# Kernel optimization log

Hardware: AMD Instinct MI355X
Metric: run time of the kernel (lower is better)

Reference implementation:

```python
import jax, jax.numpy as jnp
import numpy as np

B, N, D = 4, 8192, 3
BIG = 1e9  # large finite value to invalidate masked points in min-reduction

def setup_inputs() -> dict:
    key = jax.random.key(0)
    k1, k2, k3, k4 = jax.random.split(key, 4)
    pred = jax.random.normal(k1, (B, N, D), jnp.float32) * 0.05
    target = jax.random.normal(k2, (B, N, D), jnp.float32) * 0.05
    points = jax.random.normal(k3, (B, N, D), jnp.float32)
    mask = jax.random.randint(k4, (B, N), 0, 2).astype(jnp.int32)
    return {"pred": pred, "target": target, "mask": mask, "points": points}

def reference(pred, target, mask, points):
    m = mask.astype(pred.dtype)  # [B, N]
    # masked L1 term: per-point mean over coords, masked mean over all points
    l1 = jnp.abs(pred - target).mean(-1)          # [B, N]
    l1 = (l1 * m).sum() / m.sum()
    # Chamfer between clean and predicted denoised points (squared L2, pytorch3d norm=2)
    clean = points + target                        # [B, N, 3]
    predp = points + pred                          # [B, N, 3]
    d2 = (jnp.sum(clean * clean, -1)[:, :, None]
          + jnp.sum(predp * predp, -1)[:, None, :]
          - 2.0 * jnp.einsum('bnd,bmd->bnm', clean, predp))  # [B, N, N]
    d2 = jnp.maximum(d2, 0.0)
    inv = (1.0 - m) * BIG                          # [B, N], penalty for masked-out points
    min_x = jnp.min(d2 + inv[:, None, :], axis=2)  # [B, N] nearest pred point for each clean
    min_y = jnp.min(d2 + inv[:, :, None], axis=1)  # [B, N] nearest clean point for each pred
    count = jnp.maximum(m.sum(-1), 1.0)            # valid points per batch
    cham = (min_x * m).sum(-1) / count + (min_y * m).sum(-1) / count  # [B]
    cd = cham.sum() / B
    return 0.5 * (l1 + cd)
```

## Files before the change

### kernel.cpp

```cpp
#include <hip/hip_runtime.h>
#include <stdint.h>

#define NPTS 8192
#define BATCH 4
#define CHUNK 512

typedef __attribute__((ext_vector_type(8))) short bf16x8;
typedef __attribute__((ext_vector_type(16))) float f32x16;

struct Accum {
  float l1sum;
  float count[BATCH];
  float minsum[8];
  float pad[3];
};

__device__ __forceinline__ unsigned short f2bf(float x) {
  union { float f; unsigned u; } v; v.f = x;
  unsigned r = v.u + 0x7FFFu + ((v.u >> 16) & 1u);
  return (unsigned short)(r >> 16);
}
__device__ __forceinline__ float bf2f(unsigned short h) {
  union { float f; unsigned u; } v; v.u = ((unsigned)h) << 16;
  return v.f;
}

using as1_t = __attribute__((address_space(1))) const unsigned int;
using as3_t = __attribute__((address_space(3))) unsigned int;
__device__ __forceinline__ void lds_load16(const void* g, void* l) {
  __builtin_amdgcn_global_load_lds((as1_t*)g, (as3_t*)l, 16, 0, 0);
}

__device__ __forceinline__ void writeA(uint4* P, int T, int n,
                                       float x, float y, float z, float nn) {
  float ax = -2.f * x, ay = -2.f * y, az = -2.f * z;
  unsigned xh = f2bf(ax), xl = f2bf(ax - bf2f(xh));
  unsigned yh = f2bf(ay), yl = f2bf(ay - bf2f(yh));
  unsigned zh = f2bf(az), zl = f2bf(az - bf2f(zh));
  unsigned nh = f2bf(nn);
  float rem = nn - bf2f((unsigned short)nh);
  unsigned nm = f2bf(rem);
  unsigned nl = f2bf(rem - bf2f((unsigned short)nm));
  uint4 h0, h1;
  h0.x = xh | (xh << 16); h0.y = xl | (xl << 16);
  h0.z = yh | (yh << 16); h0.w = yl | (yl << 16);
  h1.x = zh | (zh << 16); h1.y = zl | (zl << 16);
  h1.z = nh | (nm << 16); h1.w = nl;
  P[T * 64 + n] = h0;
  P[T * 64 + 32 + n] = h1;
}
__device__ __forceinline__ void writeB(uint4* P, int T, int n,
                                       float x, float y, float z) {
  unsigned xh = f2bf(x), xl = f2bf(x - bf2f((unsigned short)xh));
  unsigned yh = f2bf(y), yl = f2bf(y - bf2f((unsigned short)yh));
  unsigned zh = f2bf(z), zl = f2bf(z - bf2f((unsigned short)zh));
  const unsigned ONE = 0x3F80u;
  unsigned ux = xh | (xl << 16), uy = yh | (yl << 16), uz = zh | (zl << 16);
  uint4 h0, h1;
  h0.x = ux; h0.y = ux; h0.z = uy; h0.w = uy;
  h1.x = uz; h1.y = uz; h1.z = ONE | (ONE << 16); h1.w = ONE;
  P[T * 64 + n] = h0;
  P[T * 64 + 32 + n] = h1;
}

__global__ __launch_bounds__(256) void prep_kernel(
    const float* __restrict__ pred, const float* __restrict__ target,
    const int* __restrict__ mask, const float* __restrict__ points,
    uint4* __restrict__ Apred, uint4* __restrict__ Aclean,
    uint4* __restrict__ Bclean, uint4* __restrict__ Bpred,
    float* __restrict__ qnClean, float* __restrict__ qnPred,
    float* __restrict__ l1part, Accum* __restrict__ acc) {
  int tid = threadIdx.x;
  int g = blockIdx.x * 256 + tid;
  if (g < 16) ((float*)acc)[g] = 0.f;
  float px = pred[3 * g], py = pred[3 * g + 1], pz = pred[3 * g + 2];
  float tx = target[3 * g], ty = target[3 * g + 1], tz = target[3 * g + 2];
  float ox = points[3 * g], oy = points[3 * g + 1], oz = points[3 * g + 2];
  int m = mask[g];
  float cx = ox + tx, cy = oy + ty, cz = oz + tz;
  float qx = ox + px, qy = oy + py, qz = oz + pz;
  float cn = cx * cx + cy * cy + cz * cz;
  float qn = qx * qx + qy * qy + qz * qz;
  float pen = m ? 0.f : 1e9f;
  qnClean[g] = cn;
  qnPred[g] = qn;
  int T = g >> 5, n = g & 31;
  writeA(Apred, T, n, qx, qy, qz, qn + pen);
  writeA(Aclean, T, n, cx, cy, cz, cn + pen);
  writeB(Bclean, T, n, cx, cy, cz);
  writeB(Bpred, T, n, qx, qy, qz);

  float fm = (float)m;
  float l1c = fm * (fabsf(px - tx) + fabsf(py - ty) + fabsf(pz - tz)) * (1.f / 3.f);
  for (int off = 32; off; off >>= 1) l1c += __shfl_down(l1c, off);
  __shared__ float pl[4];
  if ((tid & 63) == 0) pl[tid >> 6] = l1c;
  __syncthreads();
  if (tid == 0) l1part[blockIdx.x] = pl[0] + pl[1] + pl[2] + pl[3];
}

__global__ __launch_bounds__(256) void chamfer_kernel(
    const uint4* __restrict__ Apred, const uint4* __restrict__ Aclean,
    const uint4* __restrict__ Bclean, const uint4* __restrict__ Bpred,
    const float* __restrict__ qnClean, const float* __restrict__ qnPred,
    float* __restrict__ partial) {
  __shared__ uint4 Asm[1024];
  int z = blockIdx.z, dir = z >> 2, b = z & 3;
  const uint4* __restrict__ Ag = dir ? Aclean : Apred;
  const uint4* __restrict__ Bg = dir ? Bpred : Bclean;
  const float* __restrict__ qn = dir ? qnPred : qnClean;
  int jx = blockIdx.x, jbase = jx * CHUNK;
  int qbase = blockIdx.y * CHUNK;
  int tid = threadIdx.x;

  const uint4* Agp = Ag + (size_t)(b * NPTS + jbase) * 2;
#pragma unroll
  for (int it = 0; it < 4; it++) lds_load16(Agp + it * 256 + tid, &Asm[it * 256 + tid]);

  int lane = tid & 63, w = tid >> 6, n = lane & 31;
  const bf16x8* Bb = (const bf16x8*)(Bg + (size_t)(b * NPTS + qbase) * 2);
  bf16x8 bfr[4];
  float acc[4];
#pragma unroll
  for (int q = 0; q < 4; q++) {
    bfr[q] = Bb[(w * 4 + q) * 64 + lane];
    acc[q] = 1e30f;
  }
  __syncthreads();

  const bf16x8* Al = (const bf16x8*)Asm;
  f32x16 zacc = {0.f, 0.f, 0.f, 0.f, 0.f, 0.f, 0.f, 0.f,
                 0.f, 0.f, 0.f, 0.f, 0.f, 0.f, 0.f, 0.f};

#pragma unroll 4
  for (int p = 0; p < 16; p++) {
    bf16x8 af = Al[p * 64 + lane];
#pragma unroll
    for (int q = 0; q < 4; q++) {
      f32x16 d = __builtin_amdgcn_mfma_f32_32x32x16_bf16(af, bfr[q], zacc, 0, 0, 0);
      acc[q] = fminf(fminf(d[0], d[1]), acc[q]);
      acc[q] = fminf(fminf(d[2], d[3]), acc[q]);
      acc[q] = fminf(fminf(d[4], d[5]), acc[q]);
      acc[q] = fminf(fminf(d[6], d[7]), acc[q]);
      acc[q] = fminf(fminf(d[8], d[9]), acc[q]);
      acc[q] = fminf(fminf(d[10], d[11]), acc[q]);
      acc[q] = fminf(fminf(d[12], d[13]), acc[q]);
      acc[q] = fminf(fminf(d[14], d[15]), acc[q]);
    }
  }

  float* __restrict__ Pq = partial + ((size_t)(z * 16 + jx)) * NPTS + qbase;
#pragma unroll
  for (int q = 0; q < 4; q++) {
    float v = fminf(acc[q], __shfl_xor(acc[q], 32));
    int qi = (w * 4 + q) * 32 + n;
    if (lane < 32) Pq[qi] = fmaxf(v + qn[b * NPTS + qbase + qi], 0.f);
  }
}

__global__ __launch_bounds__(256) void reduce_kernel(
    const int* __restrict__ mask, const float* __restrict__ partial,
    Accum* __restrict__ acc) {
  int slice = blockIdx.x >> 3, sub = blockIdx.x & 7;
  int dir = slice >> 2, bb = slice & 3;
  int t = threadIdx.x;
  const float* __restrict__ P = partial + (size_t)slice * 16 * NPTS + sub * 1024;
  float s = 0.f, c = 0.f;
  for (int i = t; i < 1024; i += 256) {
    float v = P[i];
#pragma unroll
    for (int jxx = 1; jxx < 16; jxx++) v = fminf(v, P[jxx * NPTS + i]);
    float m = (float)mask[bb * NPTS + sub * 1024 + i];
    s += m * v;
    c += m;
  }
  for (int off = 32; off; off >>= 1) {
    s += __shfl_down(s, off);
    c += __shfl_down(c, off);
  }
  __shared__ float rs[4], rc[4];
  int wave = t >> 6;
  if ((t & 63) == 0) { rs[wave] = s; rc[wave] = c; }
  __syncthreads();
  if (t == 0) {
    atomicAdd(&acc->minsum[slice], rs[0] + rs[1] + rs[2] + rs[3]);
    if (dir == 0) atomicAdd(&acc->count[bb], rc[0] + rc[1] + rc[2] + rc[3]);
  }
}

__global__ void final_kernel(const Accum* __restrict__ acc,
                             const float* __restrict__ l1part,
                             float* __restrict__ out) {
  int t = threadIdx.x;
  float l1 = l1part[t];
  for (int off = 32; off; off >>= 1) l1 += __shfl_down(l1, off);
  __shared__ float r[2];
  if ((t & 63) == 0) r[t >> 6] = l1;
  __syncthreads();
  if (t == 0) {
    float l1s = r[0] + r[1];
    float msum = 0.f, cham = 0.f;
#pragma unroll
    for (int b = 0; b < BATCH; b++) {
      msum += acc->count[b];
      cham += (acc->minsum[b] + acc->minsum[4 + b]) / fmaxf(acc->count[b], 1.f);
    }
    out[0] = 0.5f * (l1s / msum + cham * (1.f / BATCH));
  }
}

extern "C" void kernel_launch(void* const* d_in, const int* in_sizes, int n_in,
                              void* d_out, int out_size, void* d_ws, size_t ws_size,
                              hipStream_t stream) {
  const float* pred   = (const float*)d_in[0];
  const float* target = (const float*)d_in[1];
  const int*   mask   = (const int*)d_in[2];
  const float* points = (const float*)d_in[3];
  float* out = (float*)d_out;

  const int NP = BATCH * NPTS;
  uint4* Apred  = (uint4*)d_ws;
  uint4* Aclean = Apred + NP * 2;
  uint4* Bclean = Aclean + NP * 2;
  uint4* Bpred  = Bclean + NP * 2;
  float* qnClean = (float*)(Bpred + NP * 2);
  float* qnPred  = qnClean + NP;
  float* partial = qnPred + NP;
  float* l1part  = partial + 8 * 16 * NPTS;
  Accum* acc     = (Accum*)(l1part + 128);

  prep_kernel<<<NP / 256, 256, 0, stream>>>(
      pred, target, mask, points, Apred, Aclean, Bclean, Bpred,
      qnClean, qnPred, l1part, acc);

  dim3 grid(NPTS / CHUNK, NPTS / CHUNK, 2 * BATCH);
  chamfer_kernel<<<grid, 256, 0, stream>>>(
      Apred, Aclean, Bclean, Bpred, qnClean, qnPred, partial);

  reduce_kernel<<<64, 256, 0, stream>>>(mask, partial, acc);
  final_kernel<<<1, 128, 0, stream>>>(acc, l1part, out);
}
```

Measured before the change: 93.77 us.

## Enlarge chamfer j-tile with double-buffered LDS, atomicMin partials, fuse final reduce

Measured after the change: 96.99 us. +3.4%, slower.

```diff
diff --git a/kernel.cpp b/kernel.cpp
--- a/kernel.cpp
+++ b/kernel.cpp
@@ -3,16 +3,15 @@
 
 #define NPTS 8192
 #define BATCH 4
-#define CHUNK 512
 
 typedef __attribute__((ext_vector_type(8))) short bf16x8;
 typedef __attribute__((ext_vector_type(16))) float f32x16;
 
 struct Accum {
-  float l1sum;
-  float count[BATCH];
+  float count[4];
   float minsum[8];
-  float pad[3];
+  unsigned ticket;
+  unsigned pad[3];
 };
 
 __device__ __forceinline__ unsigned short f2bf(float x) {
@@ -63,16 +62,20 @@
   P[T * 64 + 32 + n] = h1;
 }
 
-__global__ __launch_bounds__(256) void prep_kernel(
+__global__ __launch_bounds__(64) void prep_kernel(
     const float* __restrict__ pred, const float* __restrict__ target,
     const int* __restrict__ mask, const float* __restrict__ points,
     uint4* __restrict__ Apred, uint4* __restrict__ Aclean,
     uint4* __restrict__ Bclean, uint4* __restrict__ Bpred,
     float* __restrict__ qnClean, float* __restrict__ qnPred,
-    float* __restrict__ l1part, Accum* __restrict__ acc) {
+    unsigned* __restrict__ minbuf, float* __restrict__ l1part,
+    Accum* __restrict__ acc) {
   int tid = threadIdx.x;
-  int g = blockIdx.x * 256 + tid;
-  if (g < 16) ((float*)acc)[g] = 0.f;
+  int g = blockIdx.x * 64 + tid;
+  if (g < 16) ((unsigned*)acc)[g] = 0u;
+  minbuf[g] = 0x7F800000u;
+  minbuf[g + BATCH * NPTS] = 0x7F800000u;
+
   float px = pred[3 * g], py = pred[3 * g + 1], pz = pred[3 * g + 2];
   float tx = target[3 * g], ty = target[3 * g + 1], tz = target[3 * g + 2];
   float ox = points[3 * g], oy = points[3 * g + 1], oz = points[3 * g + 2];
@@ -93,27 +96,24 @@
   float fm = (float)m;
   float l1c = fm * (fabsf(px - tx) + fabsf(py - ty) + fabsf(pz - tz)) * (1.f / 3.f);
   for (int off = 32; off; off >>= 1) l1c += __shfl_down(l1c, off);
-  __shared__ float pl[4];
-  if ((tid & 63) == 0) pl[tid >> 6] = l1c;
-  __syncthreads();
-  if (tid == 0) l1part[blockIdx.x] = pl[0] + pl[1] + pl[2] + pl[3];
+  if (tid == 0) l1part[blockIdx.x] = l1c;
 }
 
 __global__ __launch_bounds__(256) void chamfer_kernel(
     const uint4* __restrict__ Apred, const uint4* __restrict__ Aclean,
     const uint4* __restrict__ Bclean, const uint4* __restrict__ Bpred,
     const float* __restrict__ qnClean, const float* __restrict__ qnPred,
-    float* __restrict__ partial) {
-  __shared__ uint4 Asm[1024];
+    unsigned* __restrict__ minbuf) {
+  __shared__ uint4 Asm[2048];
   int z = blockIdx.z, dir = z >> 2, b = z & 3;
   const uint4* __restrict__ Ag = dir ? Aclean : Apred;
   const uint4* __restrict__ Bg = dir ? Bpred : Bclean;
   const float* __restrict__ qn = dir ? qnPred : qnClean;
-  int jx = blockIdx.x, jbase = jx * CHUNK;
-  int qbase = blockIdx.y * CHUNK;
+  int jbase = blockIdx.x * 2048;
+  int qbase = blockIdx.y * 512;
   int tid = threadIdx.x;
-
   const uint4* Agp = Ag + (size_t)(b * NPTS + jbase) * 2;
+
 #pragma unroll
   for (int it = 0; it < 4; it++) lds_load16(Agp + it * 256 + tid, &Asm[it * 256 + tid]);
 
@@ -128,50 +128,62 @@
   }
   __syncthreads();
 
-  const bf16x8* Al = (const bf16x8*)Asm;
   f32x16 zacc = {0.f, 0.f, 0.f, 0.f, 0.f, 0.f, 0.f, 0.f,
                  0.f, 0.f, 0.f, 0.f, 0.f, 0.f, 0.f, 0.f};
 
+  for (int s = 0; s < 4; s++) {
+    if (s < 3) {
+      const uint4* An = Agp + (s + 1) * 1024;
+      uint4* dst = &Asm[((s + 1) & 1) * 1024];
+#pragma unroll
+      for (int it = 0; it < 4; it++) lds_load16(An + it * 256 + tid, &dst[it * 256 + tid]);
+    }
+    const bf16x8* Al = (const bf16x8*)&Asm[(s & 1) * 1024];
 #pragma unroll 4
-  for (int p = 0; p < 16; p++) {
-    bf16x8 af = Al[p * 64 + lane];
-#pragma unroll
-    for (int q = 0; q < 4; q++) {
-      f32x16 d = __builtin_amdgcn_mfma_f32_32x32x16_bf16(af, bfr[q], zacc, 0, 0, 0);
-      acc[q] = fminf(fminf(d[0], d[1]), acc[q]);
-      acc[q] = fminf(fminf(d[2], d[3]), acc[q]);
-      acc[q] = fminf(fminf(d[4], d[5]), acc[q]);
-      acc[q] = fminf(fminf(d[6], d[7]), acc[q]);
-      acc[q] = fminf(fminf(d[8], d[9]), acc[q]);
-      acc[q] = fminf(fminf(d[10], d[11]), acc[q]);
-      acc[q] = fminf(fminf(d[12], d[13]), acc[q]);
-      acc[q] = fminf(fminf(d[14], d[15]), acc[q]);
-    }
-  }
-
-  float* __restrict__ Pq = partial + ((size_t)(z * 16 + jx)) * NPTS + qbase;
+    for (int p = 0; p < 16; p++) {
+      bf16x8 af = Al[p * 64 + lane];
+#pragma unroll
+      for (int q = 0; q < 4; q++) {
+        f32x16 d = __builtin_amdgcn_mfma_f32_32x32x16_bf16(af, bfr[q], zacc, 0, 0, 0);
+        acc[q] = fminf(fminf(d[0], d[1]), acc[q]);
+        acc[q] = fminf(fminf(d[2], d[3]), acc[q]);
+        acc[q] = fminf(fminf(d[4], d[5]), acc[q]);
+        acc[q] = fminf(fminf(d[6], d[7]), acc[q]);
+        acc[q] = fminf(fminf(d[8], d[9]), acc[q]);
+        acc[q] = fminf(fminf(d[10], d[11]), acc[q]);
+        acc[q] = fminf(fminf(d[12], d[13]), acc[q]);
+        acc[q] = fminf(fminf(d[14], d[15]), acc[q]);
+      }
+    }
+    __syncthreads();
+  }
+
+  unsigned* __restrict__ Mq = minbuf + (size_t)z * NPTS + qbase;
 #pragma unroll
   for (int q = 0; q < 4; q++) {
     float v = fminf(acc[q], __shfl_xor(acc[q], 32));
     int qi = (w * 4 + q) * 32 + n;
-    if (lane < 32) Pq[qi] = fmaxf(v + qn[b * NPTS + qbase + qi], 0.f);
+    if (lane < 32) {
+      float r = fmaxf(v + qn[b * NPTS + qbase + qi], 0.f);
+      atomicMin(&Mq[qi], __float_as_uint(r));
+    }
   }
 }
 
 __global__ __launch_bounds__(256) void reduce_kernel(
-    const int* __restrict__ mask, const float* __restrict__ partial,
-    Accum* __restrict__ acc) {
-  int slice = blockIdx.x >> 3, sub = blockIdx.x & 7;
+    const int* __restrict__ mask, const unsigned* __restrict__ minbuf,
+    const float* __restrict__ l1part, Accum* __restrict__ acc,
+    float* __restrict__ out) {
+  int blk = blockIdx.x;
+  int slice = blk >> 3, sub = blk & 7;
   int dir = slice >> 2, bb = slice & 3;
   int t = threadIdx.x;
-  const float* __restrict__ P = partial + (size_t)slice * 16 * NPTS + sub * 1024;
+  const unsigned* __restrict__ P = minbuf + (size_t)slice * NPTS + sub * 1024;
+  const int* __restrict__ M = mask + bb * NPTS + sub * 1024;
   float s = 0.f, c = 0.f;
   for (int i = t; i < 1024; i += 256) {
-    float v = P[i];
-#pragma unroll
-    for (int jxx = 1; jxx < 16; jxx++) v = fminf(v, P[jxx * NPTS + i]);
-    float m = (float)mask[bb * NPTS + sub * 1024 + i];
-    s += m * v;
+    float m = (float)M[i];
+    s += m * __uint_as_float(P[i]);
     c += m;
   }
   for (int off = 32; off; off >>= 1) {
@@ -179,31 +191,35 @@
     c += __shfl_down(c, off);
   }
   __shared__ float rs[4], rc[4];
-  int wave = t >> 6;
-  if ((t & 63) == 0) { rs[wave] = s; rc[wave] = c; }
+  __shared__ int lastf;
+  int wv = t >> 6;
+  if ((t & 63) == 0) { rs[wv] = s; rc[wv] = c; }
   __syncthreads();
   if (t == 0) {
     atomicAdd(&acc->minsum[slice], rs[0] + rs[1] + rs[2] + rs[3]);
     if (dir == 0) atomicAdd(&acc->count[bb], rc[0] + rc[1] + rc[2] + rc[3]);
-  }
-}
-
-__global__ void final_kernel(const Accum* __restrict__ acc,
-                             const float* __restrict__ l1part,
-                             float* __restrict__ out) {
-  int t = threadIdx.x;
-  float l1 = l1part[t];
+    __threadfence();
+    unsigned tk = atomicAdd(&acc->ticket, 1u);
+    lastf = (tk == 63u);
+    if (tk == 63u) __threadfence();
+  }
+  __syncthreads();
+  if (!lastf) return;
+
+  float l1 = l1part[t] + l1part[t + 256];
   for (int off = 32; off; off >>= 1) l1 += __shfl_down(l1, off);
-  __shared__ float r[2];
-  if ((t & 63) == 0) r[t >> 6] = l1;
+  __shared__ float rl[4];
+  if ((t & 63) == 0) rl[t >> 6] = l1;
   __syncthreads();
   if (t == 0) {
-    float l1s = r[0] + r[1];
+    float l1s = rl[0] + rl[1] + rl[2] + rl[3];
+    volatile float* va = (volatile float*)acc;
     float msum = 0.f, cham = 0.f;
 #pragma unroll
     for (int b = 0; b < BATCH; b++) {
-      msum += acc->count[b];
-      cham += (acc->minsum[b] + acc->minsum[4 + b]) / fmaxf(acc->count[b], 1.f);
+      float cb = va[b];
+      msum += cb;
+      cham += (va[4 + b] + va[8 + b]) / fmaxf(cb, 1.f);
     }
     out[0] = 0.5f * (l1s / msum + cham * (1.f / BATCH));
   }
@@ -225,18 +241,17 @@
   uint4* Bpred  = Bclean + NP * 2;
   float* qnClean = (float*)(Bpred + NP * 2);
   float* qnPred  = qnClean + NP;
-  float* partial = qnPred + NP;
-  float* l1part  = partial + 8 * 16 * NPTS;
-  Accum* acc     = (Accum*)(l1part + 128);
-
-  prep_kernel<<<NP / 256, 256, 0, stream>>>(
+  unsigned* minbuf = (unsigned*)(qnPred + NP);
+  float* l1part  = (float*)(minbuf + 2 * NP);
+  Accum* acc     = (Accum*)(l1part + 512);
+
+  prep_kernel<<<NP / 64, 64, 0, stream>>>(
       pred, target, mask, points, Apred, Aclean, Bclean, Bpred,
-      qnClean, qnPred, l1part, acc);
-
-  dim3 grid(NPTS / CHUNK, NPTS / CHUNK, 2 * BATCH);
+      qnClean, qnPred, minbuf, l1part, acc);
+
+  dim3 grid(4, NPTS / 512, 2 * BATCH);
   chamfer_kernel<<<grid, 256, 0, stream>>>(
-      Apred, Aclean, Bclean, Bpred, qnClean, qnPred, partial);
-
-  reduce_kernel<<<64, 256, 0, stream>>>(mask, partial, acc);
-  final_kernel<<<1, 128, 0, stream>>>(acc, l1part, out);
-}
+      Apred, Aclean, Bclean, Bpred, qnClean, qnPred, minbuf);
+
+  reduce_kernel<<<64, 256, 0, stream>>>(mask, minbuf, l1part, acc, out);
+}
```
